# Performance work log

Hardware: AMD Instinct MI355X
Metric: run time of the kernel (lower is better)

## Reference

```python
import jax, jax.numpy as jnp
import numpy as np

DT = 0.05      # bsde.delta_t
EPS = 1e-6     # BatchNormalization epsilon


def _bn(x, gamma, beta):
    # training-mode batch norm: statistics over the batch axis
    m = jnp.mean(x, axis=0, keepdims=True)
    v = jnp.var(x, axis=0, keepdims=True)
    return (x - m) * jax.lax.rsqrt(v + EPS) * gamma + beta


def _subnet(x, g0, b0, W0, g1, b1, W1, g2, b2, W2, bias2, g3, b3):
    # bn -> (dense -> bn -> relu) x 2 -> dense(+bias) -> bn
    x = _bn(x, g0, b0)
    x = jax.nn.relu(_bn(x @ W0, g1, b1))
    x = jax.nn.relu(_bn(x @ W1, g2, b2))
    x = _bn(x @ W2 + bias2, g3, b3)
    return x


def setup_inputs() -> dict:
    key = jax.random.key(0)
    B, D, N, H = 8192, 100, 20, 110
    T = N - 1  # number of subnets
    ks = jax.random.split(key, 18)
    u = lambda k, s, lo, hi: jax.random.uniform(k, s, jnp.float32, lo, hi)
    s_dh = np.sqrt(2.0 / (D + H)).astype(np.float32)
    s_hh = np.sqrt(2.0 / (H + H)).astype(np.float32)
    s_hd = np.sqrt(2.0 / (H + D)).astype(np.float32)
    return {
        "dw": jax.random.normal(ks[0], (B, D, N), jnp.float32) * np.sqrt(DT).astype(np.float32),
        "x": jax.random.normal(ks[1], (B, D, N + 1), jnp.float32),
        "mean_y_input": jax.random.normal(ks[2], (N,), jnp.float32),
        "y_init": u(ks[3], (1,), 0.0, 1.0),
        "z_init": u(ks[4], (1, D), -0.1, 0.1),
        "gamma0": u(ks[5], (T, D), 0.1, 0.5),
        "beta0": 0.1 * jax.random.normal(ks[6], (T, D), jnp.float32),
        "W0": s_dh * jax.random.normal(ks[7], (T, D, H), jnp.float32),
        "gamma1": u(ks[8], (T, H), 0.1, 0.5),
        "beta1": 0.1 * jax.random.normal(ks[9], (T, H), jnp.float32),
        "W1": s_hh * jax.random.normal(ks[10], (T, H, H), jnp.float32),
        "gamma2": u(ks[11], (T, H), 0.1, 0.5),
        "beta2": 0.1 * jax.random.normal(ks[12], (T, H), jnp.float32),
        "W2": s_hd * jax.random.normal(ks[13], (T, H, D), jnp.float32),
        "bias2": jnp.zeros((T, D), jnp.float32),
        "gamma3": u(ks[14], (T, D), 0.1, 0.5),
        "beta3": 0.1 * jax.random.normal(ks[15], (T, D), jnp.float32),
    }


def reference(dw, x, mean_y_input, y_init, z_init, gamma0, beta0, W0,
              gamma1, beta1, W1, gamma2, beta2, W2, bias2, gamma3, beta3):
    B, D, N = dw.shape
    T = N - 1
    # z at step t+1 depends only on x[:, :, t+1] and subnet t -> compute all in parallel
    x_steps = jnp.moveaxis(x[:, :, 1:N], 2, 0)  # [T, B, D]
    z_all = jax.vmap(_subnet)(x_steps, gamma0, beta0, W0, gamma1, beta1, W1,
                              gamma2, beta2, W2, bias2, gamma3, beta3) / D  # [T, B, D]
    z0 = jnp.broadcast_to(z_init, (B, D))          # all_one_vec @ z_init
    zs = jnp.concatenate([z0[None], z_all], axis=0)  # [N, B, D] (z used at each update)
    dw_steps = jnp.moveaxis(dw, 2, 0)               # [N, B, D]
    y0 = jnp.ones((B, 1), dw.dtype) * y_init

    def step(y, zd):
        z, dwt = zd
        # f_tf(t, x, y, z) = sin(y) for the SineBM equation
        y_new = y - DT * jnp.sin(y) + jnp.sum(z * dwt, axis=1, keepdims=True)
        return y_new, jnp.mean(y_new)

    y_final, means = jax.lax.scan(step, y0, (zs, dw_steps))
    mean_y = jnp.concatenate([jnp.mean(y0)[None], means[:T]])  # length N
    return y_final, mean_y
```

## Files before the change

kernel.cpp:

```cpp
#include <hip/hip_runtime.h>

typedef unsigned short u16;
typedef unsigned int   u32;

#define BATCH  8192
#define DIM    100
#define HID    110
#define TSUB   19
#define NSTEP  20
#define KP     128
#define NPAD   112
#define BN_EPS 1e-6f
#define DT_C   0.05f

#define SAB  2048
#define SAR  (BATCH / SAB)
#define SLICES 32
#define NBLK_SCAN 2048

typedef __bf16 v8bf __attribute__((ext_vector_type(8)));
typedef float  v4f  __attribute__((ext_vector_type(4)));
typedef float  v2f  __attribute__((ext_vector_type(2)));
typedef u16    u16x4 __attribute__((ext_vector_type(4)));

__device__ __forceinline__ u16 f2bf(float f) {
    u32 u = __float_as_uint(f);
    return (u16)((u + 0x7fffu + ((u >> 16) & 1u)) >> 16);
}
__device__ __forceinline__ float bf2f(u16 h) {
    return __uint_as_float(((u32)h) << 16);
}
__device__ __forceinline__ void acc4(float4& s, float4& q, float4 v) {
    s.x += v.x; s.y += v.y; s.z += v.z; s.w += v.w;
    q.x += v.x * v.x; q.y += v.y * v.y; q.z += v.z * v.z; q.w += v.w * v.w;
}

__global__ void statsA(const float* __restrict__ x, float* __restrict__ part,
                       u32* __restrict__ xT32) {
    __shared__ u16 xls[SAR][2112];
    const int tid = threadIdx.x;
    const int b0 = blockIdx.x * SAR;
    float4 s0 = {0,0,0,0}, q0 = {0,0,0,0};
    float4 s1 = {0,0,0,0}, q1 = {0,0,0,0};
    float4 s2 = {0,0,0,0}, q2 = {0,0,0,0};
#pragma unroll
    for (int r = 0; r < SAR; r++) {
        const float4* row = (const float4*)(x + (size_t)(b0 + r) * 2100);
        float4 v0 = row[tid];
        float4 v1 = row[tid + 256];
        acc4(s0, q0, v0);
        acc4(s1, q1, v1);
        u16x4 p0 = { f2bf(v0.x), f2bf(v0.y), f2bf(v0.z), f2bf(v0.w) };
        u16x4 p1 = { f2bf(v1.x), f2bf(v1.y), f2bf(v1.z), f2bf(v1.w) };
        *(u16x4*)&xls[r][tid * 4]        = p0;
        *(u16x4*)&xls[r][1024 + tid * 4] = p1;
        if (tid < 13) {
            float4 v2 = row[tid + 512];
            acc4(s2, q2, v2);
            u16x4 p2 = { f2bf(v2.x), f2bf(v2.y), f2bf(v2.z), f2bf(v2.w) };
            *(u16x4*)&xls[r][2048 + tid * 4] = p2;
        }
    }
    float* ps = part + (size_t)blockIdx.x * 4200;
    *(float4*)&ps[tid * 4]               = s0;
    *(float4*)&ps[1024 + tid * 4]        = s1;
    *(float4*)&ps[2100 + tid * 4]        = q0;
    *(float4*)&ps[2100 + 1024 + tid * 4] = q1;
    if (tid < 13) {
        *(float4*)&ps[2048 + tid * 4]        = s2;
        *(float4*)&ps[2100 + 2048 + tid * 4] = q2;
    }
    __syncthreads();
    const int TOT = TSUB * SAR * (NPAD / 2);
    for (int i = tid; i < TOT; i += 256) {
        int w = i % (NPAD / 2);
        int seg = i / (NPAD / 2);
        int r = seg % SAR, t = seg / SAR;
        int d0 = w * 2;
        u32 v = 0;
        if (d0 < DIM) {
            u16 lo = xls[r][d0 * 21 + t + 1];
            u16 hi = (d0 + 1 < DIM) ? xls[r][(d0 + 1) * 21 + t + 1] : (u16)0;
            v = (u32)lo | ((u32)hi << 16);
        }
        xT32[((size_t)t * BATCH + b0 + r) * (NPAD / 2) + w] = v;
    }
}

__global__ void statsB(const float* __restrict__ part, float* __restrict__ out) {
    int gid = blockIdx.x * 256 + threadIdx.x;
    if (gid >= 4200 * SLICES) return;
    int slice = gid / 4200;
    int o = gid - slice * 4200;
    const float* p = part + (size_t)slice * (SAB / SLICES) * 4200 + o;
    float acc = 0.f;
#pragma unroll 8
    for (int i = 0; i < SAB / SLICES; i++) acc += p[(size_t)i * 4200];
    atomicAdd(&out[o], acc);
}

__global__ void wtrans(const float* __restrict__ W0, const float* __restrict__ W1,
                       const float* __restrict__ W2, u16* __restrict__ WTsw) {
    __shared__ float lw[HID * HID];
    const int t = blockIdx.x, l = blockIdx.y, tid = threadIdx.x;
    const float* W; int K, N;
    if (l == 0)      { W = W0; K = DIM; N = HID; }
    else if (l == 1) { W = W1; K = HID; N = HID; }
    else             { W = W2; K = HID; N = DIM; }
    const float* Wt = W + (size_t)t * K * N;
    for (int i = tid; i < K * N; i += 256) lw[i] = Wt[i];
    __syncthreads();
    u16* out = WTsw + ((size_t)l * TSUB + t) * (NPAD * KP);
    for (int i = tid; i < NPAD * 16; i += 256) {
        int n = i / 16, p = i % 16;
        int kc = p ^ (n & 7);
        u16 o8[8];
#pragma unroll
        for (int j = 0; j < 8; j++) {
            int k = kc * 8 + j;
            float v = (k < K && n < N) ? lw[k * N + n] : 0.f;
            o8[j] = f2bf(v);
        }
        *(uint4*)&out[(size_t)n * KP + p * 8] = *(uint4*)o8;
    }
}

template <int KREAL, int NOUT, int IDXMODE, int RELU, int BMAJOR>
__global__ __launch_bounds__(512, 2)
void gemm_kernel(const u16* __restrict__ Ain,
                 const u16* __restrict__ WTswL,
                 const float* __restrict__ sumIn,
                 const float* __restrict__ sqIn,
                 const float* __restrict__ gIn,
                 const float* __restrict__ bIn,
                 u16* __restrict__ Hout,
                 float* __restrict__ sumArr,
                 float* __restrict__ sqArr) {
    __shared__ __align__(16) u16 Alds[128 * KP];
    __shared__ __align__(16) u16 Blds[NPAD * KP];
    __shared__ float s_sum[NPAD], s_sq[NPAD];
    __shared__ float aAffL[KP], cAffL[KP];

    const int tid = threadIdx.x;
    const int mt = blockIdx.x;
    const int t  = blockIdx.y;
    const int brow0 = mt * 128;

    if (tid < NPAD) { s_sum[tid] = 0.f; s_sq[tid] = 0.f; }
    if (tid < KREAL) {
        int idx = (IDXMODE == 0) ? (tid * 21 + (t + 1)) : (t * KREAL + tid);
        float m = sumIn[idx] * (1.f / BATCH);
        float v = sqIn[idx] * (1.f / BATCH) - m * m;
        float rstd = rsqrtf(v + BN_EPS);
        float ga = gIn[t * KREAL + tid] * rstd;
        aAffL[tid] = ga;
        cAffL[tid] = bIn[t * KREAL + tid] - m * ga;
    }

    {
        const uint4* wsrc = (const uint4*)(WTswL + (size_t)t * NPAD * KP);
        uint4* bl = (uint4*)Blds;
        for (int i = tid; i < NPAD * KP / 8; i += 512) bl[i] = wsrc[i];
    }
    const int NCH = (KREAL + 7) / 8;
    for (int i = tid; i < 128 * (16 - NCH); i += 512) {
        int row = i / (16 - NCH);
        int kc  = NCH + i % (16 - NCH);
        uint4 z = {0, 0, 0, 0};
        *(uint4*)&Alds[row * KP + (kc ^ (row & 7)) * 8] = z;
    }
    __syncthreads();

    for (int cidx = tid; cidx < 128 * NCH; cidx += 512) {
        int row = cidx / NCH;
        int kc  = cidx % NCH;
        int k0  = kc * 8;
        const u16* hrow = Ain + ((size_t)t * BATCH + brow0 + row) * NPAD + k0;
        u16 hv[8];
        *(uint4*)hv = *(const uint4*)hrow;
        u16 pk[8];
#pragma unroll
        for (int j = 0; j < 8; j++) {
            int k = k0 + j;
            float av = (k < KREAL) ? fmaf(bf2f(hv[j]), aAffL[k], cAffL[k]) : 0.f;
            if (RELU) av = fmaxf(av, 0.f);
            pk[j] = f2bf(av);
        }
        *(uint4*)&Alds[row * KP + ((kc ^ (row & 7)) * 8)] = *(uint4*)pk;
    }
    __syncthreads();

    const int lane = tid & 63;
    const int wv   = tid >> 6;
    const int r0   = lane & 15;
    const int q    = lane >> 4;
    const int moff = wv * 16;

    v4f acc[7];
#pragma unroll
    for (int j = 0; j < 7; j++) { v4f z = {0.f, 0.f, 0.f, 0.f}; acc[j] = z; }

#pragma unroll
    for (int ks = 0; ks < 4; ks++) {
        int cbase = ks * 4 + q;
        int row = moff + r0;
        v8bf afr = *(const v8bf*)&Alds[row * KP + ((cbase ^ (row & 7)) * 8)];
#pragma unroll
        for (int nf = 0; nf < 7; nf++) {
            int nr = nf * 16 + r0;
            v8bf bfr = *(const v8bf*)&Blds[nr * KP + ((cbase ^ (nr & 7)) * 8)];
            acc[nf] = __builtin_amdgcn_mfma_f32_16x16x32_bf16(afr, bfr, acc[nf], 0, 0, 0);
        }
    }

#pragma unroll
    for (int nf = 0; nf < 7; nf++) {
        int n = nf * 16 + r0;
#pragma unroll
        for (int rg = 0; rg < 4; rg++) {
            int grow = brow0 + moff + q * 4 + rg;
            size_t oidx = BMAJOR ? ((size_t)grow * (TSUB * NPAD) + (size_t)t * NPAD + n)
                                 : (((size_t)t * BATCH + grow) * NPAD + n);
            Hout[oidx] = f2bf(acc[nf][rg]);
        }
    }
#pragma unroll
    for (int nf = 0; nf < 7; nf++) {
        float cs = 0.f, cq = 0.f;
#pragma unroll
        for (int rg = 0; rg < 4; rg++) {
            float vv = acc[nf][rg];
            cs += vv; cq += vv * vv;
        }
        cs += __shfl_xor(cs, 16); cs += __shfl_xor(cs, 32);
        cq += __shfl_xor(cq, 16); cq += __shfl_xor(cq, 32);
        if (q == 0) {
            atomicAdd(&s_sum[nf * 16 + r0], cs);
            atomicAdd(&s_sq[nf * 16 + r0], cq);
        }
    }
    __syncthreads();
    if (tid < NOUT) {
        atomicAdd(&sumArr[t * NOUT + tid], s_sum[tid]);
        atomicAdd(&sqArr[t * NOUT + tid], s_sq[tid]);
    }
}

__global__ void finalize3(const float* __restrict__ sum3, const float* __restrict__ sq3,
                          const float* __restrict__ g3, const float* __restrict__ b3,
                          float4* __restrict__ acg) {
    int i = blockIdx.x * 256 + threadIdx.x;
    if (i >= TSUB * 50) return;
    int t = i / 50, p = i - t * 50;
    int e = t * DIM + 2 * p;
    float4 o;
#pragma unroll
    for (int h = 0; h < 2; h++) {
        float m = sum3[e + h] * (1.f / BATCH);
        float v = sq3[e + h] * (1.f / BATCH) - m * m;
        float rstd = rsqrtf(v + BN_EPS);
        float ga = g3[e + h] * rstd * (1.f / DIM);
        float cc = b3[e + h] * (1.f / DIM) - m * ga;
        if (h == 0) { o.x = ga; o.y = cc; } else { o.z = ga; o.w = cc; }
    }
    acg[i] = o;
}

__global__ __launch_bounds__(256, 4)
void scan_kernel(const float* __restrict__ dw,
                 const u16* __restrict__ zbuf,
                 const float4* __restrict__ acg,
                 const float* __restrict__ z_init, const float* __restrict__ y_init,
                 float* __restrict__ yout, float* __restrict__ mred) {
    __shared__ float bsum[NSTEP];
    const int tid = threadIdx.x;
    if (tid < NSTEP) bsum[tid] = 0.f;
    __syncthreads();

    const int wv = tid >> 6, lane = tid & 63;
    const int b = blockIdx.x * 4 + wv;
    const int ll = (lane < 50) ? lane : 49;

    v4f w[10];
    u32 zr[TSUB];
    v2f zi;
    {
        const float* dwaddr = dw + (size_t)b * (DIM * NSTEP) + ll * 40;
        const u16*   zaddr  = zbuf + (size_t)b * (TSUB * NPAD) + 2 * ll;
        const float* ziaddr = z_init + 2 * ll;
        asm volatile("global_load_dwordx4 %0, %1, off offset:0"   : "=v"(w[0]) : "v"(dwaddr));
        asm volatile("global_load_dwordx4 %0, %1, off offset:16"  : "=v"(w[1]) : "v"(dwaddr));
        asm volatile("global_load_dwordx4 %0, %1, off offset:32"  : "=v"(w[2]) : "v"(dwaddr));
        asm volatile("global_load_dwordx4 %0, %1, off offset:48"  : "=v"(w[3]) : "v"(dwaddr));
        asm volatile("global_load_dwordx4 %0, %1, off offset:64"  : "=v"(w[4]) : "v"(dwaddr));
        asm volatile("global_load_dwordx4 %0, %1, off offset:80"  : "=v"(w[5]) : "v"(dwaddr));
        asm volatile("global_load_dwordx4 %0, %1, off offset:96"  : "=v"(w[6]) : "v"(dwaddr));
        asm volatile("global_load_dwordx4 %0, %1, off offset:112" : "=v"(w[7]) : "v"(dwaddr));
        asm volatile("global_load_dwordx4 %0, %1, off offset:128" : "=v"(w[8]) : "v"(dwaddr));
        asm volatile("global_load_dwordx4 %0, %1, off offset:144" : "=v"(w[9]) : "v"(dwaddr));
#pragma unroll
        for (int t = 0; t < TSUB; t++)
            asm volatile("global_load_dword %0, %1, off offset:%2"
                         : "=v"(zr[t]) : "v"(zaddr), "i"(t * NPAD * 2));
        asm volatile("global_load_dwordx2 %0, %1, off" : "=v"(zi) : "v"(ziaddr));
        asm volatile("s_waitcnt vmcnt(0)" ::: "memory");
        __builtin_amdgcn_sched_barrier(0);
    }

    float acc[NSTEP];
#pragma unroll
    for (int k = 0; k < NSTEP; k++) acc[k] = 0.f;
    if (lane < 50) {
        acc[0] = zi[0] * w[0][0] + zi[1] * w[5][0];
#pragma unroll
        for (int t = 0; t < TSUB; t++) {
            float4 ac = acg[t * 50 + ll];
            u32 z = zr[t];
            float za0 = fmaf(bf2f((u16)(z & 0xffffu)), ac.x, ac.y);
            float za1 = fmaf(bf2f((u16)(z >> 16)),     ac.z, ac.w);
            const int n = t + 1, j = n >> 2, k = n & 3;
            acc[n] += w[j][k] * za0 + w[5 + j][k] * za1;
        }
    }

#pragma unroll
    for (int m = 1; m < 64; m <<= 1) {
#pragma unroll
        for (int k = 0; k < NSTEP; k++) acc[k] += __shfl_xor(acc[k], m, 64);
    }

    const float yi = y_init[0];
    float y = yi, ysave = 0.f;
#pragma unroll
    for (int i = 0; i < NSTEP; i++) {
        y = y - DT_C * __sinf(y) + acc[i];
        if (i == lane - 1) ysave = y;
    }
    if (lane == 0) yout[b] = y;
    if (lane >= 1 && lane < NSTEP) atomicAdd(&bsum[lane], ysave);
    __syncthreads();
    if (tid >= 1 && tid < NSTEP) mred[blockIdx.x * NSTEP + tid] = bsum[tid];
}

__global__ void meanred(const float* __restrict__ mred, const float* __restrict__ y_init,
                        float* __restrict__ meanout) {
    const int n = blockIdx.x, tid = threadIdx.x;
    if (n == 0) { if (tid == 0) meanout[0] = y_init[0]; return; }
    float s = 0.f;
    for (int i = tid; i < NBLK_SCAN; i += 256) s += mred[(size_t)i * NSTEP + n];
#pragma unroll
    for (int m = 1; m < 64; m <<= 1) s += __shfl_xor(s, m, 64);
    __shared__ float ws4[4];
    if ((tid & 63) == 0) ws4[tid >> 6] = s;
    __syncthreads();
    if (tid == 0) meanout[n] = (ws4[0] + ws4[1] + ws4[2] + ws4[3]) * (1.f / BATCH);
}

extern "C" void kernel_launch(void* const* d_in, const int* in_sizes, int n_in,
                              void* d_out, int out_size, void* d_ws, size_t ws_size,
                              hipStream_t stream) {
    const float* dw     = (const float*)d_in[0];
    const float* x      = (const float*)d_in[1];
    const float* y_init = (const float*)d_in[3];
    const float* z_init = (const float*)d_in[4];
    const float* g0 = (const float*)d_in[5];
    const float* b0 = (const float*)d_in[6];
    const float* W0 = (const float*)d_in[7];
    const float* g1 = (const float*)d_in[8];
    const float* b1 = (const float*)d_in[9];
    const float* W1 = (const float*)d_in[10];
    const float* g2 = (const float*)d_in[11];
    const float* b2 = (const float*)d_in[12];
    const float* W2 = (const float*)d_in[13];
    const float* g3 = (const float*)d_in[15];
    const float* b3 = (const float*)d_in[16];

    char* ws = (char*)d_ws;
    size_t off = 0;
    auto alloc = [&](size_t bytes) -> void* {
        off = (off + 255) & ~(size_t)255;
        void* p = ws + off;
        off += bytes;
        return p;
    };

    const int nStats = 4200 + TSUB * HID * 2 * 2 + TSUB * DIM * 2;
    float* statsBlk = (float*)alloc((size_t)nStats * 4);
    float* sum0 = statsBlk;            float* sq0  = sum0 + 2100;
    float* sum1 = sum0 + 4200;         float* sq1  = sum1 + TSUB * HID;
    float* sum2 = sq1 + TSUB * HID;    float* sq2  = sum2 + TSUB * HID;
    float* sum3 = sq2 + TSUB * HID;    float* sq3  = sum3 + TSUB * DIM;

    u16* WTsw = (u16*)alloc((size_t)3 * TSUB * NPAD * KP * 2);
    float4* acg = (float4*)alloc((size_t)TSUB * 50 * 16);
    float* mred = (float*)alloc((size_t)NBLK_SCAN * NSTEP * 4);

    const size_t hBytes = (size_t)TSUB * BATCH * NPAD * 2;
    u16* h0 = (u16*)alloc(hBytes);
    u16* h1 = (u16*)alloc(hBytes);
    u16* outbuf = h0;
    float* part = (float*)h0;
    u32*  xT32  = (u32*)h1;

    float* yout = (float*)d_out;
    float* meanout = yout + BATCH;

    hipMemsetAsync(statsBlk, 0, (size_t)nStats * 4, stream);

    wtrans<<<dim3(TSUB, 3), 256, 0, stream>>>(W0, W1, W2, WTsw);
    statsA<<<SAB, 256, 0, stream>>>(x, part, xT32);
    statsB<<<(4200 * SLICES + 255) / 256, 256, 0, stream>>>(part, sum0);

    const u16* xT = (const u16*)xT32;
    u16* WT0 = WTsw;
    u16* WT1 = WTsw + (size_t)TSUB * NPAD * KP;
    u16* WT2 = WTsw + (size_t)2 * TSUB * NPAD * KP;

    gemm_kernel<DIM, HID, 0, 0, 0><<<dim3(64, TSUB), 512, 0, stream>>>(xT, WT0, sum0, sq0, g0, b0, h0, sum1, sq1);
    gemm_kernel<HID, HID, 1, 1, 0><<<dim3(64, TSUB), 512, 0, stream>>>(h0, WT1, sum1, sq1, g1, b1, h1, sum2, sq2);
    gemm_kernel<HID, DIM, 1, 1, 1><<<dim3(64, TSUB), 512, 0, stream>>>(h1, WT2, sum2, sq2, g2, b2, outbuf, sum3, sq3);

    finalize3<<<4, 256, 0, stream>>>(sum3, sq3, g3, b3, acg);
    scan_kernel<<<NBLK_SCAN, 256, 0, stream>>>(dw, outbuf, acg, z_init, y_init, yout, mred);
    meanred<<<NSTEP, 256, 0, stream>>>(mred, y_init, meanout);
}
```

Baseline: 183.9 us.

## Load GEMM A operands straight into registers and fold first BN scale into W0

The A tile is no longer staged through LDS. Each lane loads its bf16 row chunks from global memory into registers and applies the batch-norm affine and ReLU there before the MFMAs. For the first layer, a new scaleW0 kernel folds the input batch-norm scale into the transposed W0. The shift term is dropped, since a per-column constant is removed by the following batch norm's mean subtraction. Freeing the 32KB A buffer lets launch bounds rise to 4 blocks per CU, at the cost of uncoalesced per-lane global loads and some extra bf16 rounding from pre-scaling the weights.

```diff
diff --git a/kernel.cpp b/kernel.cpp
--- a/kernel.cpp
+++ b/kernel.cpp
@@ -125,8 +125,34 @@
     }
 }
 
-template <int KREAL, int NOUT, int IDXMODE, int RELU, int BMAJOR>
-__global__ __launch_bounds__(512, 2)
+__global__ void scaleW0(const float* __restrict__ sum0, const float* __restrict__ sq0,
+                        const float* __restrict__ g0, u16* __restrict__ WT0) {
+    __shared__ float aL[DIM];
+    const int t = blockIdx.x, tid = threadIdx.x;
+    if (tid < DIM) {
+        int idx = tid * 21 + (t + 1);
+        float m = sum0[idx] * (1.f / BATCH);
+        float v = sq0[idx] * (1.f / BATCH) - m * m;
+        aL[tid] = g0[t * DIM + tid] * rsqrtf(v + BN_EPS);
+    }
+    __syncthreads();
+    u16* wt = WT0 + (size_t)t * NPAD * KP;
+    for (int i = tid; i < NPAD * 16; i += 256) {
+        int n = i >> 4, p = i & 15;
+        int kc = p ^ (n & 7);
+        uint4 v4 = *(uint4*)&wt[(size_t)n * KP + p * 8];
+        u16* e = (u16*)&v4;
+#pragma unroll
+        for (int j = 0; j < 8; j++) {
+            int k = kc * 8 + j;
+            if (k < DIM) e[j] = f2bf(bf2f(e[j]) * aL[k]);
+        }
+        *(uint4*)&wt[(size_t)n * KP + p * 8] = v4;
+    }
+}
+
+template <int KREAL, int NOUT, int AFFINE, int RELU, int BMAJOR>
+__global__ __launch_bounds__(512, 4)
 void gemm_kernel(const u16* __restrict__ Ain,
                  const u16* __restrict__ WTswL,
                  const float* __restrict__ sumIn,
@@ -136,7 +162,6 @@
                  u16* __restrict__ Hout,
                  float* __restrict__ sumArr,
                  float* __restrict__ sqArr) {
-    __shared__ __align__(16) u16 Alds[128 * KP];
     __shared__ __align__(16) u16 Blds[NPAD * KP];
     __shared__ float s_sum[NPAD], s_sq[NPAD];
     __shared__ float aAffL[KP], cAffL[KP];
@@ -147,14 +172,17 @@
     const int brow0 = mt * 128;
 
     if (tid < NPAD) { s_sum[tid] = 0.f; s_sq[tid] = 0.f; }
-    if (tid < KREAL) {
-        int idx = (IDXMODE == 0) ? (tid * 21 + (t + 1)) : (t * KREAL + tid);
-        float m = sumIn[idx] * (1.f / BATCH);
-        float v = sqIn[idx] * (1.f / BATCH) - m * m;
-        float rstd = rsqrtf(v + BN_EPS);
-        float ga = gIn[t * KREAL + tid] * rstd;
-        aAffL[tid] = ga;
-        cAffL[tid] = bIn[t * KREAL + tid] - m * ga;
+    if (AFFINE) {
+        if (tid >= KREAL && tid < KP) { aAffL[tid] = 0.f; cAffL[tid] = 0.f; }
+        if (tid < KREAL) {
+            int idx = t * KREAL + tid;
+            float m = sumIn[idx] * (1.f / BATCH);
+            float v = sqIn[idx] * (1.f / BATCH) - m * m;
+            float rstd = rsqrtf(v + BN_EPS);
+            float ga = gIn[idx] * rstd;
+            aAffL[tid] = ga;
+            cAffL[tid] = bIn[idx] - m * ga;
+        }
     }
 
     {
@@ -162,54 +190,53 @@
         uint4* bl = (uint4*)Blds;
         for (int i = tid; i < NPAD * KP / 8; i += 512) bl[i] = wsrc[i];
     }
-    const int NCH = (KREAL + 7) / 8;
-    for (int i = tid; i < 128 * (16 - NCH); i += 512) {
-        int row = i / (16 - NCH);
-        int kc  = NCH + i % (16 - NCH);
-        uint4 z = {0, 0, 0, 0};
-        *(uint4*)&Alds[row * KP + (kc ^ (row & 7)) * 8] = z;
-    }
-    __syncthreads();
-
-    for (int cidx = tid; cidx < 128 * NCH; cidx += 512) {
-        int row = cidx / NCH;
-        int kc  = cidx % NCH;
-        int k0  = kc * 8;
-        const u16* hrow = Ain + ((size_t)t * BATCH + brow0 + row) * NPAD + k0;
-        u16 hv[8];
-        *(uint4*)hv = *(const uint4*)hrow;
-        u16 pk[8];
-#pragma unroll
-        for (int j = 0; j < 8; j++) {
-            int k = k0 + j;
-            float av = (k < KREAL) ? fmaf(bf2f(hv[j]), aAffL[k], cAffL[k]) : 0.f;
-            if (RELU) av = fmaxf(av, 0.f);
-            pk[j] = f2bf(av);
-        }
-        *(uint4*)&Alds[row * KP + ((kc ^ (row & 7)) * 8)] = *(uint4*)pk;
-    }
     __syncthreads();
 
     const int lane = tid & 63;
     const int wv   = tid >> 6;
     const int r0   = lane & 15;
     const int q    = lane >> 4;
-    const int moff = wv * 16;
+    const int row  = wv * 16 + r0;
+
+    const u16* arow = Ain + ((size_t)t * BATCH + brow0 + row) * NPAD;
+    u16 hv[4][8];
+#pragma unroll
+    for (int ks = 0; ks < 4; ks++) {
+        int cb = ks * 4 + q;
+        int cbl = (cb > 13) ? 13 : cb;
+        *(uint4*)hv[ks] = *(const uint4*)(arow + cbl * 8);
+    }
+    v8bf afr[4];
+#pragma unroll
+    for (int ks = 0; ks < 4; ks++) {
+        if (AFFINE) {
+            int cb = ks * 4 + q;
+            const float* ap = &aAffL[cb * 8];
+            const float* cp = &cAffL[cb * 8];
+            u16 pk[8];
+#pragma unroll
+            for (int j = 0; j < 8; j++) {
+                float av = fmaf(bf2f(hv[ks][j]), ap[j], cp[j]);
+                if (RELU) av = fmaxf(av, 0.f);
+                pk[j] = f2bf(av);
+            }
+            afr[ks] = *(v8bf*)pk;
+        } else {
+            afr[ks] = *(v8bf*)hv[ks];
+        }
+    }
 
     v4f acc[7];
 #pragma unroll
     for (int j = 0; j < 7; j++) { v4f z = {0.f, 0.f, 0.f, 0.f}; acc[j] = z; }
-
 #pragma unroll
     for (int ks = 0; ks < 4; ks++) {
         int cbase = ks * 4 + q;
-        int row = moff + r0;
-        v8bf afr = *(const v8bf*)&Alds[row * KP + ((cbase ^ (row & 7)) * 8)];
 #pragma unroll
         for (int nf = 0; nf < 7; nf++) {
             int nr = nf * 16 + r0;
             v8bf bfr = *(const v8bf*)&Blds[nr * KP + ((cbase ^ (nr & 7)) * 8)];
-            acc[nf] = __builtin_amdgcn_mfma_f32_16x16x32_bf16(afr, bfr, acc[nf], 0, 0, 0);
+            acc[nf] = __builtin_amdgcn_mfma_f32_16x16x32_bf16(afr[ks], bfr, acc[nf], 0, 0, 0);
         }
     }
 
@@ -218,7 +245,7 @@
         int n = nf * 16 + r0;
 #pragma unroll
         for (int rg = 0; rg < 4; rg++) {
-            int grow = brow0 + moff + q * 4 + rg;
+            int grow = brow0 + wv * 16 + q * 4 + rg;
             size_t oidx = BMAJOR ? ((size_t)grow * (TSUB * NPAD) + (size_t)t * NPAD + n)
                                  : (((size_t)t * BATCH + grow) * NPAD + n);
             Hout[oidx] = f2bf(acc[nf][rg]);
@@ -416,6 +443,8 @@
     u16* WT1 = WTsw + (size_t)TSUB * NPAD * KP;
     u16* WT2 = WTsw + (size_t)2 * TSUB * NPAD * KP;
 
+    scaleW0<<<TSUB, 256, 0, stream>>>(sum0, sq0, g0, WT0);
+
     gemm_kernel<DIM, HID, 0, 0, 0><<<dim3(64, TSUB), 512, 0, stream>>>(xT, WT0, sum0, sq0, g0, b0, h0, sum1, sq1);
     gemm_kernel<HID, HID, 1, 1, 0><<<dim3(64, TSUB), 512, 0, stream>>>(h0, WT1, sum1, sq1, g1, b1, h1, sum2, sq2);
     gemm_kernel<HID, DIM, 1, 1, 1><<<dim3(64, TSUB), 512, 0, stream>>>(h1, WT2, sum2, sq2, g2, b2, outbuf, sum3, sq3);
```

Measured after the change: 166.4 us. -9.5%, faster.
